# Kernel optimization log

Measured on AMD Instinct MI355X. Metric: run time of the kernel, lower is better.

Reference implementation:

```python
import jax, jax.numpy as jnp
import numpy as np

D_MODEL = 1024
EXPAND = 2
D_EXPAND = D_MODEL * EXPAND  # 2048
D_STATE = 16
DT_RANK = -(-D_MODEL // 16)  # ceil = 64
BATCH = 4
SEQ = 1024


def setup_inputs() -> dict:
    key = jax.random.key(0)
    ks = jax.random.split(key, 9)
    s = 0.02
    x = jax.random.normal(ks[0], (BATCH, SEQ, D_MODEL), dtype=jnp.float32)
    W_in = jax.random.normal(ks[1], (2 * D_EXPAND, D_MODEL), dtype=jnp.float32) * s
    conv_w = jax.random.normal(ks[2], (D_EXPAND, 1, 3), dtype=jnp.float32) * 0.3  # depthwise kernel (O, I/g=1, K)
    conv_b = jax.random.normal(ks[3], (D_EXPAND,), dtype=jnp.float32) * s
    W_xproj = jax.random.normal(ks[4], (2 * D_STATE + DT_RANK, D_EXPAND), dtype=jnp.float32) * s
    dt_std = DT_RANK ** (-0.5) * 0.5
    W_dt = jax.random.uniform(ks[5], (D_EXPAND, DT_RANK), dtype=jnp.float32, minval=-dt_std, maxval=dt_std)
    b_dt = jax.random.normal(ks[6], (D_EXPAND,), dtype=jnp.float32) * s
    A_log = jnp.log(jnp.tile(jnp.arange(1, D_STATE + 1, dtype=jnp.float32), (D_EXPAND, 1)))
    D = jnp.ones((D_EXPAND,), dtype=jnp.float32)
    W_out = jax.random.normal(ks[7], (D_MODEL, D_EXPAND), dtype=jnp.float32) * s
    return {"x": x, "W_in": W_in, "conv_w": conv_w, "conv_b": conv_b,
            "W_xproj": W_xproj, "W_dt": W_dt, "b_dt": b_dt,
            "A_log": A_log, "D": D, "W_out": W_out}


def _mamba_forward(x, W_in, conv_w, conv_b, W_xproj, W_dt, b_dt, A_log, D, W_out):
    B, L, _ = x.shape
    d_exp = D.shape[0]
    n = A_log.shape[1]
    # in_proj -> split into u (ssm branch) and z (gate)
    xz = x @ W_in.T                               # [B, L, 2*d_exp]
    u, z = jnp.split(xz, 2, axis=-1)              # each [B, L, d_exp]
    # depthwise conv1d, kernel 3, padding 1 (same length)
    uc = jax.lax.conv_general_dilated(
        u.transpose(0, 2, 1), conv_w, window_strides=(1,), padding=[(1, 1)],
        feature_group_count=d_exp, dimension_numbers=("NCH", "OIH", "NCH"))
    uc = jax.nn.silu(uc + conv_b[None, :, None]).transpose(0, 2, 1)  # [B, L, d_exp]
    # ssm parameterization
    proj = uc @ W_xproj.T                          # [B, L, 2n + dt_rank]
    B_ssm = proj[..., :n]                          # [B, L, n]
    C_ssm = proj[..., n:2 * n]                     # [B, L, n]
    dt = proj[..., 2 * n:]                         # [B, L, dt_rank]
    delta = jax.nn.softplus(dt @ W_dt.T + b_dt)    # [B, L, d_exp]
    A = -jnp.exp(A_log)                            # [d_exp, n]

    def step(h, inp):
        u_t, d_t, b_t, c_t = inp                   # [B,d], [B,d], [B,n], [B,n]
        dA = jnp.exp(d_t[:, :, None] * A)          # [B, d, n]
        h = dA * h + (d_t * u_t)[:, :, None] * b_t[:, None, :]
        y_t = jnp.einsum("bdn,bn->bd", h, c_t)
        return h, y_t

    xs = (uc.transpose(1, 0, 2), delta.transpose(1, 0, 2),
          B_ssm.transpose(1, 0, 2), C_ssm.transpose(1, 0, 2))
    h0 = jnp.zeros((B, d_exp, n), dtype=uc.dtype)
    _, ys = jax.lax.scan(step, h0, xs)             # ys: [L, B, d_exp]
    y = ys.transpose(1, 0, 2) + uc * D             # skip connection D
    y = y * jax.nn.silu(z)                         # gate
    return y @ W_out.T                             # [B, L, d_model]


def reference(x, W_in, conv_w, conv_b, W_xproj, W_dt, b_dt, A_log, D, W_out):
    return _mamba_forward(x, W_in, conv_w, conv_b, W_xproj, W_dt, b_dt, A_log, D, W_out)
```

## Files before the change

kernel.cpp:

```cpp
#include <hip/hip_runtime.h>
#include <math.h>

#define B_   4
#define L_   1024
#define DM   1024
#define DE   2048
#define NS   16
#define M_   (B_*L_)
#define NC   32
#define CL   32

typedef __attribute__((ext_vector_type(8))) short bf16x8;
typedef __attribute__((ext_vector_type(4))) float f32x4;

#define AS1 __attribute__((address_space(1)))
#define AS3 __attribute__((address_space(3)))

__device__ __forceinline__ void gload_lds16(const void* g, void* l) {
  __builtin_amdgcn_global_load_lds((const AS1 unsigned int*)g,
                                   (AS3 unsigned int*)l, 16, 0, 0);
}

__device__ __forceinline__ unsigned short f2bf(float f) {
  unsigned int u = __builtin_bit_cast(unsigned int, f);
  u = (u + 0x7fffu + ((u >> 16) & 1u)) >> 16;
  return (unsigned short)u;
}
__device__ __forceinline__ float bf2f(unsigned short h) {
  unsigned int u = ((unsigned int)h) << 16;
  return __builtin_bit_cast(float, u);
}
__device__ __forceinline__ float fexp2(float x) {
  return __builtin_amdgcn_exp2f(x);
}

__global__ __launch_bounds__(256)
void convert_all_k(const float* __restrict__ x, const float* __restrict__ Win,
                   const float* __restrict__ Wout, const float* __restrict__ Wx,
                   unsigned short* __restrict__ x_bf, unsigned short* __restrict__ Win_bf,
                   unsigned short* __restrict__ Wout_bf, unsigned short* __restrict__ Wxp) {
  const int blk = blockIdx.x;
  const float* src; unsigned short* dst; size_t base; bool pad = false;
  if (blk < 2048)      { src = x;    dst = x_bf;    base = (size_t)blk * 2048; }
  else if (blk < 4096) { src = Win;  dst = Win_bf;  base = (size_t)(blk - 2048) * 2048; }
  else if (blk < 5120) { src = Wout; dst = Wout_bf; base = (size_t)(blk - 4096) * 2048; }
  else                 { src = Wx;   dst = Wxp;     base = (size_t)(blk - 5120) * 2048; pad = true; }
  const size_t i = base + (size_t)threadIdx.x * 8;
  unsigned short o[8] = {0,0,0,0,0,0,0,0};
  if (!pad || (int)(i >> 11) < 96) {
    float4 a = *(const float4*)(src + i);
    float4 b = *(const float4*)(src + i + 4);
    o[0]=f2bf(a.x); o[1]=f2bf(a.y); o[2]=f2bf(a.z); o[3]=f2bf(a.w);
    o[4]=f2bf(b.x); o[5]=f2bf(b.y); o[6]=f2bf(b.z); o[7]=f2bf(b.w);
  }
  *(ulonglong2*)(dst + i) = *(const ulonglong2*)o;
}

__global__ __launch_bounds__(256, 2)
void gemm1_k(const unsigned short* __restrict__ A, const unsigned short* __restrict__ Bt,
             unsigned short* __restrict__ C) {
  __shared__ unsigned short Asl[256 * 32];
  __shared__ unsigned short Bsl[128 * 32];
  const int tid  = threadIdx.x;
  const int lane = tid & 63;
  const int wave = tid >> 6;
  const int row0 = blockIdx.y * 256, col0 = blockIdx.x * 128;
  const int wr = (wave >> 1) * 128, wc = (wave & 1) * 64;

  const unsigned short* AgP[4];
  #pragma unroll
  for (int g = 0; g < 4; ++g) {
    const int c = g * 256 + tid;
    AgP[g] = A + (size_t)(row0 + (c >> 2)) * DM + ((c & 3) << 3);
  }
  const unsigned short* BgP[2];
  #pragma unroll
  for (int g = 0; g < 2; ++g) {
    const int c = g * 256 + tid;
    BgP[g] = Bt + (size_t)(col0 + (c >> 2)) * DM + ((c & 3) << 3);
  }

  const int frow = lane & 15;
  const int fk   = (lane >> 4) << 3;
  const unsigned short* Afr = Asl + ((wr + frow) << 5) + fk;
  const unsigned short* Bfr = Bsl + ((wc + frow) << 5) + fk;

  f32x4 acc[8][4];
  #pragma unroll
  for (int m = 0; m < 8; ++m)
    #pragma unroll
    for (int n = 0; n < 4; ++n) acc[m][n] = (f32x4){0.f, 0.f, 0.f, 0.f};

  for (int k0 = 0; k0 < DM; k0 += 32) {
    __syncthreads();
    #pragma unroll
    for (int g = 0; g < 4; ++g)
      gload_lds16(AgP[g] + k0, Asl + (((g << 8) + (wave << 6)) << 3));
    #pragma unroll
    for (int g = 0; g < 2; ++g)
      gload_lds16(BgP[g] + k0, Bsl + (((g << 8) + (wave << 6)) << 3));
    __syncthreads();
    bf16x8 af[8], bfr[4];
    #pragma unroll
    for (int m = 0; m < 8; ++m) af[m]  = *(const bf16x8*)(Afr + (m << 9));
    #pragma unroll
    for (int n = 0; n < 4; ++n) bfr[n] = *(const bf16x8*)(Bfr + (n << 9));
    #pragma unroll
    for (int m = 0; m < 8; ++m)
      #pragma unroll
      for (int n = 0; n < 4; ++n)
        acc[m][n] = __builtin_amdgcn_mfma_f32_16x16x32_bf16(af[m], bfr[n], acc[m][n], 0, 0, 0);
  }

  const int r4 = (lane >> 4) << 2;
  #pragma unroll
  for (int m = 0; m < 8; ++m)
    #pragma unroll
    for (int n = 0; n < 4; ++n) {
      unsigned short* Cp = C + (size_t)(row0 + wr + m * 16 + r4) * 4096 + col0 + wc + n * 16 + (lane & 15);
      #pragma unroll
      for (int r = 0; r < 4; ++r) Cp[(size_t)r * 4096] = f2bf(acc[m][n][r]);
    }
}

__global__ __launch_bounds__(256)
void gemm2_k(const unsigned short* __restrict__ A, const unsigned short* __restrict__ Bt,
             float* __restrict__ C) {
  __shared__ unsigned short Asl[128 * 32];
  __shared__ unsigned short Bsl[64 * 32];
  const int tid  = threadIdx.x;
  const int lane = tid & 63;
  const int wave = tid >> 6;
  const int row0 = blockIdx.y * 128, col0 = blockIdx.x * 64;
  const int wr = (wave >> 1) * 64, wc = (wave & 1) * 32;

  const int c0 = tid, c1 = 256 + tid;
  const unsigned short* Ag0 = A + (size_t)(row0 + (c0 >> 2)) * DE + ((c0 & 3) << 3);
  const unsigned short* Ag1 = A + (size_t)(row0 + (c1 >> 2)) * DE + ((c1 & 3) << 3);
  const unsigned short* Bg0 = Bt + (size_t)(col0 + (c0 >> 2)) * DE + ((c0 & 3) << 3);
  unsigned short* Al0 = Asl + ((wave << 6) << 3);
  unsigned short* Al1 = Asl + ((256 + (wave << 6)) << 3);
  unsigned short* Bl0 = Bsl + ((wave << 6) << 3);

  const int frow = lane & 15;
  const int fk   = (lane >> 4) << 3;
  const unsigned short* Afr = Asl + ((wr + frow) << 5) + fk;
  const unsigned short* Bfr = Bsl + ((wc + frow) << 5) + fk;

  f32x4 acc[4][2];
  #pragma unroll
  for (int m = 0; m < 4; ++m)
    #pragma unroll
    for (int n = 0; n < 2; ++n) acc[m][n] = (f32x4){0.f, 0.f, 0.f, 0.f};

  for (int k0 = 0; k0 < DE; k0 += 32) {
    __syncthreads();
    gload_lds16(Ag0 + k0, Al0);
    gload_lds16(Ag1 + k0, Al1);
    gload_lds16(Bg0 + k0, Bl0);
    __syncthreads();
    bf16x8 af[4], bfr[2];
    #pragma unroll
    for (int m = 0; m < 4; ++m) af[m]  = *(const bf16x8*)(Afr + (m << 9));
    #pragma unroll
    for (int n = 0; n < 2; ++n) bfr[n] = *(const bf16x8*)(Bfr + (n << 9));
    #pragma unroll
    for (int m = 0; m < 4; ++m)
      #pragma unroll
      for (int n = 0; n < 2; ++n)
        acc[m][n] = __builtin_amdgcn_mfma_f32_16x16x32_bf16(af[m], bfr[n], acc[m][n], 0, 0, 0);
  }

  const int r4 = (lane >> 4) << 2;
  #pragma unroll
  for (int m = 0; m < 4; ++m)
    #pragma unroll
    for (int n = 0; n < 2; ++n) {
      float* Cp = C + (size_t)(row0 + wr + m * 16 + r4) * DM + col0 + wc + n * 16 + (lane & 15);
      #pragma unroll
      for (int r = 0; r < 4; ++r) Cp[(size_t)r * DM] = acc[m][n][r];
    }
}

__global__ __launch_bounds__(256)
void proj_gemm_k(const unsigned short* __restrict__ A,
                 const unsigned short* __restrict__ Bt,
                 float* __restrict__ part) {
  __shared__ unsigned short Asl[128 * 32];
  __shared__ unsigned short Bsl[128 * 32];
  const int tid  = threadIdx.x;
  const int lane = tid & 63;
  const int wave = tid >> 6;
  const int ks   = blockIdx.x;
  const int row0 = blockIdx.y * 128;
  const int wr = (wave >> 1) * 64, wc = (wave & 1) * 64;
  const int kbase = ks * 256;

  const int c0 = tid, c1 = 256 + tid;
  const unsigned short* Ag0 = A + (size_t)(row0 + (c0 >> 2)) * DE + ((c0 & 3) << 3) + kbase;
  const unsigned short* Ag1 = A + (size_t)(row0 + (c1 >> 2)) * DE + ((c1 & 3) << 3) + kbase;
  const unsigned short* Bg0 = Bt + (size_t)(c0 >> 2) * DE + ((c0 & 3) << 3) + kbase;
  const unsigned short* Bg1 = Bt + (size_t)(c1 >> 2) * DE + ((c1 & 3) << 3) + kbase;
  unsigned short* Al0 = Asl + ((wave << 6) << 3);
  unsigned short* Al1 = Asl + ((256 + (wave << 6)) << 3);
  unsigned short* Bl0 = Bsl + ((wave << 6) << 3);
  unsigned short* Bl1 = Bsl + ((256 + (wave << 6)) << 3);

  const int frow = lane & 15;
  const int fk   = (lane >> 4) << 3;
  const unsigned short* Afr = Asl + ((wr + frow) << 5) + fk;
  const unsigned short* Bfr = Bsl + ((wc + frow) << 5) + fk;

  f32x4 acc[4][4];
  #pragma unroll
  for (int m = 0; m < 4; ++m)
    #pragma unroll
    for (int n = 0; n < 4; ++n) acc[m][n] = (f32x4){0.f, 0.f, 0.f, 0.f};

  for (int k0 = 0; k0 < 256; k0 += 32) {
    __syncthreads();
    gload_lds16(Ag0 + k0, Al0);
    gload_lds16(Ag1 + k0, Al1);
    gload_lds16(Bg0 + k0, Bl0);
    gload_lds16(Bg1 + k0, Bl1);
    __syncthreads();
    bf16x8 af[4], bfr[4];
    #pragma unroll
    for (int m = 0; m < 4; ++m) af[m]  = *(const bf16x8*)(Afr + (m << 9));
    #pragma unroll
    for (int n = 0; n < 4; ++n) bfr[n] = *(const bf16x8*)(Bfr + (n << 9));
    #pragma unroll
    for (int m = 0; m < 4; ++m)
      #pragma unroll
      for (int n = 0; n < 4; ++n)
        acc[m][n] = __builtin_amdgcn_mfma_f32_16x16x32_bf16(af[m], bfr[n], acc[m][n], 0, 0, 0);
  }

  float* Cb = part + (size_t)ks * (M_ * 128) + (size_t)row0 * 128;
  const int r4 = (lane >> 4) << 2;
  #pragma unroll
  for (int m = 0; m < 4; ++m)
    #pragma unroll
    for (int n = 0; n < 4; ++n) {
      float* Cp = Cb + (size_t)(wr + m * 16 + r4) * 128 + wc + n * 16 + (lane & 15);
      #pragma unroll
      for (int r = 0; r < 4; ++r) Cp[(size_t)r * 128] = acc[m][n][r];
    }
}

__global__ __launch_bounds__(256)
void proj_reduce_k(const float* __restrict__ part, float* __restrict__ proj) {
  const int g = blockIdx.x * 256 + threadIdx.x;
  const int m = g / 24;
  const int j4 = (g - m * 24) * 4;
  float4 s = make_float4(0.f, 0.f, 0.f, 0.f);
  #pragma unroll
  for (int ks = 0; ks < 8; ++ks) {
    float4 v = *(const float4*)(part + (size_t)ks * (M_ * 128) + (size_t)m * 128 + j4);
    s.x += v.x; s.y += v.y; s.z += v.z; s.w += v.w;
  }
  *(float4*)(proj + (size_t)m * 96 + j4) = s;
}

__global__ __launch_bounds__(256)
void conv_silu_k(const unsigned short* __restrict__ xz, const float* __restrict__ cw,
                 const float* __restrict__ cb, unsigned short* __restrict__ uc_bf) {
  const int g = blockIdx.x * 256 + threadIdx.x;
  const int m = g >> 9;
  const int d4 = (g & 511) << 2;
  const int l = m & (L_ - 1);
  const unsigned short* row = xz + (size_t)m * 4096 + d4;
  unsigned short cu[4], pv[4] = {0,0,0,0}, nx[4] = {0,0,0,0};
  *(unsigned long long*)cu = *(const unsigned long long*)row;
  if (l > 0)      *(unsigned long long*)pv = *(const unsigned long long*)(row - 4096);
  if (l < L_ - 1) *(unsigned long long*)nx = *(const unsigned long long*)(row + 4096);
  unsigned short ob[4];
  #pragma unroll
  for (int i = 0; i < 4; ++i) {
    const int d = d4 + i;
    float v = cb[d] + cw[d*3]*bf2f(pv[i]) + cw[d*3+1]*bf2f(cu[i]) + cw[d*3+2]*bf2f(nx[i]);
    ob[i] = f2bf(v / (1.f + __expf(-v)));
  }
  *(unsigned long long*)(uc_bf + (size_t)m * DE + d4) = *(const unsigned long long*)ob;
}

__global__ __launch_bounds__(256)
void delta_k(const float* __restrict__ proj, const float* __restrict__ Wdt,
             const float* __restrict__ bdt, unsigned short* __restrict__ dl) {
  __shared__ float As[64][64];
  __shared__ float Bs[64][64];
  const int tid = threadIdx.x;
  const int row0 = blockIdx.y * 64, col0 = blockIdx.x * 64;
  const int ty = tid >> 4, tx = tid & 15;
  #pragma unroll
  for (int q = 0; q < 4; ++q) {
    const int f = q*256 + tid;
    const int rr = f >> 4, cc = (f & 15) << 2;
    float4 v = *(const float4*)(proj + (size_t)(row0+rr)*96 + 32 + cc);
    As[cc+0][rr]=v.x; As[cc+1][rr]=v.y; As[cc+2][rr]=v.z; As[cc+3][rr]=v.w;
    float4 w = *(const float4*)(Wdt + (size_t)(col0+rr)*64 + cc);
    Bs[cc+0][rr]=w.x; Bs[cc+1][rr]=w.y; Bs[cc+2][rr]=w.z; Bs[cc+3][rr]=w.w;
  }
  __syncthreads();
  float acc[4][4];
  #pragma unroll
  for (int i = 0; i < 4; ++i)
    #pragma unroll
    for (int j = 0; j < 4; ++j) acc[i][j] = 0.f;
  #pragma unroll 8
  for (int k = 0; k < 64; ++k) {
    const float4 a = *(const float4*)&As[k][ty*4];
    const float4 w = *(const float4*)&Bs[k][tx*4];
    const float a_[4]={a.x,a.y,a.z,a.w}, b_[4]={w.x,w.y,w.z,w.w};
    #pragma unroll
    for (int i = 0; i < 4; ++i)
      #pragma unroll
      for (int j = 0; j < 4; ++j)
        acc[i][j] = fmaf(a_[i], b_[j], acc[i][j]);
  }
  #pragma unroll
  for (int i = 0; i < 4; ++i) {
    const int m = row0 + ty*4 + i;
    unsigned short ob[4];
    #pragma unroll
    for (int j = 0; j < 4; ++j) {
      const float v = acc[i][j] + bdt[col0 + tx*4 + j];
      ob[j] = f2bf(fmaxf(v, 0.f) + __logf(1.f + __expf(-fabsf(v))));
    }
    *(unsigned long long*)(dl + (size_t)m*DE + col0 + tx*4) = *(const unsigned long long*)ob;
  }
}

__global__ __launch_bounds__(256)
void scan_part1(const unsigned short* __restrict__ dl, const unsigned short* __restrict__ uc,
                const float* __restrict__ proj, const float* __restrict__ Alog,
                float* __restrict__ hX, float* __restrict__ sumdv) {
  __shared__ float Bsh[CL][NS];
  const int tid = threadIdx.x;
  const int d = blockIdx.x * 256 + tid;
  const int c = blockIdx.y;
  const int b = blockIdx.z;
  const size_t mt0 = (size_t)b * L_ + c * CL;
  if (tid < CL * NS / 4) {
    const int t = tid >> 2, n4 = (tid & 3) * 4;
    float4 v = *(const float4*)(proj + (mt0 + t) * 96 + n4);
    Bsh[t][n4] = v.x; Bsh[t][n4+1] = v.y; Bsh[t][n4+2] = v.z; Bsh[t][n4+3] = v.w;
  }
  float An2[NS];
  #pragma unroll
  for (int q = 0; q < 4; ++q) {
    float4 a = *(const float4*)(Alog + d * NS + q * 4);
    An2[q*4+0] = -__expf(a.x) * 1.44269504f;
    An2[q*4+1] = -__expf(a.y) * 1.44269504f;
    An2[q*4+2] = -__expf(a.z) * 1.44269504f;
    An2[q*4+3] = -__expf(a.w) * 1.44269504f;
  }
  __syncthreads();
  float h[NS];
  #pragma unroll
  for (int n = 0; n < NS; ++n) h[n] = 0.f;
  float sd = 0.f;
  size_t off = mt0 * DE + d;
  float dv = bf2f(dl[off]), uv = bf2f(uc[off]);
  for (int t = 0; t < CL; ++t) {
    float dvn = 0.f, uvn = 0.f;
    if (t + 1 < CL) { dvn = bf2f(dl[off + DE]); uvn = bf2f(uc[off + DE]); }
    sd += dv;
    const float du = dv * uv;
    #pragma unroll
    for (int n = 0; n < NS; ++n) {
      const float dA = fexp2(dv * An2[n]);
      h[n] = fmaf(dA, h[n], du * Bsh[t][n]);
    }
    dv = dvn; uv = uvn; off += DE;
  }
  const size_t xb = (size_t)(b * NC + c) * NS * DE + d;
  #pragma unroll
  for (int n = 0; n < NS; ++n) hX[xb + (size_t)n * DE] = h[n];
  sumdv[(size_t)(b * NC + c) * DE + d] = sd;
}

__global__ __launch_bounds__(256)
void scan_combine(float* __restrict__ hX, const float* __restrict__ sumdv,
                  const float* __restrict__ Alog) {
  const int tid = threadIdx.x;
  const int d = blockIdx.x * 256 + tid;
  const int n = blockIdx.y;
  const int b = blockIdx.z;
  const float An2 = -__expf(Alog[d * NS + n]) * 1.44269504f;
  float H = 0.f;
  for (int c = 0; c < NC; ++c) {
    const size_t xi = ((size_t)(b * NC + c) * NS + n) * DE + d;
    const float hf = hX[xi];
    const float sd = sumdv[(size_t)(b * NC + c) * DE + d];
    hX[xi] = H;
    H = fmaf(fexp2(sd * An2), H, hf);
  }
}

__global__ __launch_bounds__(256)
void scan_part2(const unsigned short* __restrict__ dl, const unsigned short* __restrict__ uc,
                const float* __restrict__ proj, const float* __restrict__ hX,
                const float* __restrict__ Alog, const float* __restrict__ Dv,
                const unsigned short* __restrict__ xz, unsigned short* __restrict__ ybf) {
  __shared__ float Bsh[CL][NS];
  __shared__ float Csh[CL][NS];
  const int tid = threadIdx.x;
  const int d = blockIdx.x * 256 + tid;
  const int c = blockIdx.y;
  const int b = blockIdx.z;
  const size_t mt0 = (size_t)b * L_ + c * CL;
  if (tid < 128) {
    const int t = tid >> 2, n4 = (tid & 3) * 4;
    float4 v = *(const float4*)(proj + (mt0 + t) * 96 + n4);
    Bsh[t][n4] = v.x; Bsh[t][n4+1] = v.y; Bsh[t][n4+2] = v.z; Bsh[t][n4+3] = v.w;
  } else {
    const int u = tid - 128;
    const int t = u >> 2, n4 = (u & 3) * 4;
    float4 v = *(const float4*)(proj + (mt0 + t) * 96 + 16 + n4);
    Csh[t][n4] = v.x; Csh[t][n4+1] = v.y; Csh[t][n4+2] = v.z; Csh[t][n4+3] = v.w;
  }
  float An2[NS];
  #pragma unroll
  for (int q = 0; q < 4; ++q) {
    float4 a = *(const float4*)(Alog + d * NS + q * 4);
    An2[q*4+0] = -__expf(a.x) * 1.44269504f;
    An2[q*4+1] = -__expf(a.y) * 1.44269504f;
    An2[q*4+2] = -__expf(a.z) * 1.44269504f;
    An2[q*4+3] = -__expf(a.w) * 1.44269504f;
  }
  const float Dd = Dv[d];
  float h[NS];
  const size_t xb = (size_t)(b * NC + c) * NS * DE + d;
  #pragma unroll
  for (int n = 0; n < NS; ++n) h[n] = hX[xb + (size_t)n * DE];
  __syncthreads();
  size_t off = mt0 * DE + d;
  size_t zoff = mt0 * 4096 + d + 2048;
  float dv = bf2f(dl[off]), uv = bf2f(uc[off]);
  for (int t = 0; t < CL; ++t) {
    float dvn = 0.f, uvn = 0.f;
    if (t + 1 < CL) { dvn = bf2f(dl[off + DE]); uvn = bf2f(uc[off + DE]); }
    const float zv = bf2f(xz[zoff]);
    const float du = dv * uv;
    float y = 0.f;
    #pragma unroll
    for (int n = 0; n < NS; ++n) {
      const float dA = fexp2(dv * An2[n]);
      h[n] = fmaf(dA, h[n], du * Bsh[t][n]);
      y = fmaf(h[n], Csh[t][n], y);
    }
    y = fmaf(uv, Dd, y);
    const float sz = zv / (1.f + __expf(-zv));
    ybf[off] = f2bf(y * sz);
    dv = dvn; uv = uvn; off += DE; zoff += 4096;
  }
}

extern "C" void kernel_launch(void* const* d_in, const int* in_sizes, int n_in,
                              void* d_out, int out_size, void* d_ws, size_t ws_size,
                              hipStream_t stream) {
  const float* x    = (const float*)d_in[0];
  const float* Win  = (const float*)d_in[1];
  const float* cw   = (const float*)d_in[2];
  const float* cb   = (const float*)d_in[3];
  const float* Wx   = (const float*)d_in[4];
  const float* Wdt  = (const float*)d_in[5];
  const float* bdt  = (const float*)d_in[6];
  const float* Alog = (const float*)d_in[7];
  const float* Dv   = (const float*)d_in[8];
  const float* Wout = (const float*)d_in[9];
  float* out = (float*)d_out;
  float* ws  = (float*)d_ws;

  unsigned short* xz_bf   = (unsigned short*)(ws);
  float*          proj    = ws + 8388608;
  float*          hX      = ws + 8781824;
  float*          part    = hX;
  float*          sumdv   = ws + 12976128;
  unsigned short* x_bf    = (unsigned short*)(ws + 13238272);
  unsigned short* Win_bf  = (unsigned short*)(ws + 15335424);
  unsigned short* Wout_bf = (unsigned short*)(ws + 17432576);
  unsigned short* Wxp_bf  = (unsigned short*)(ws + 18481152);
  unsigned short* uc_bf   = (unsigned short*)(ws + 18612224);
  unsigned short* y_bf    = uc_bf;
  unsigned short* dl_bf   = (unsigned short*)(ws + 22806528);

  convert_all_k<<<5248, 256, 0, stream>>>(x, Win, Wout, Wx, x_bf, Win_bf, Wout_bf, Wxp_bf);
  gemm1_k<<<dim3(32, 16), 256, 0, stream>>>(x_bf, Win_bf, xz_bf);
  conv_silu_k<<<8192, 256, 0, stream>>>(xz_bf, cw, cb, uc_bf);
  proj_gemm_k<<<dim3(8, 32), 256, 0, stream>>>(uc_bf, Wxp_bf, part);
  proj_reduce_k<<<384, 256, 0, stream>>>(part, proj);
  delta_k<<<dim3(32, 64), 256, 0, stream>>>(proj, Wdt, bdt, dl_bf);
  scan_part1<<<dim3(DE/256, NC, B_), 256, 0, stream>>>(dl_bf, uc_bf, proj, Alog, hX, sumdv);
  scan_combine<<<dim3(DE/256, NS, B_), 256, 0, stream>>>(hX, sumdv, Alog);
  scan_part2<<<dim3(DE/256, NC, B_), 256, 0, stream>>>(dl_bf, uc_bf, proj, hX, Alog, Dv, xz_bf, y_bf);
  gemm2_k<<<dim3(16, 32), 256, 0, stream>>>(y_bf, Wout_bf, out);
}
```

Before: 206.6 us.

## Double GEMM K-tile to 64 with XOR-swizzled LDS and split scan reduction

In both bf16 MFMA GEMMs, each K tile grows from 32 to 64 elements, so each block runs half as many barrier-separated load/compute iterations. The LDS layout is XOR-swizzled on 16-byte chunks by row, which is meant to avoid bank conflicts on the fragment reads. The scan kernel splits the y dot product across four partial accumulators to shorten its dependent FMA chain. The cost is twice the LDS per block, which may lower occupancy in gemm1 since it requests 2 blocks per CU.

```diff
diff --git a/kernel.cpp b/kernel.cpp
--- a/kernel.cpp
+++ b/kernel.cpp
@@ -59,31 +59,32 @@
 __global__ __launch_bounds__(256, 2)
 void gemm1_k(const unsigned short* __restrict__ A, const unsigned short* __restrict__ Bt,
              unsigned short* __restrict__ C) {
-  __shared__ unsigned short Asl[256 * 32];
-  __shared__ unsigned short Bsl[128 * 32];
+  __shared__ unsigned short Asl[256 * 64];
+  __shared__ unsigned short Bsl[128 * 64];
   const int tid  = threadIdx.x;
   const int lane = tid & 63;
   const int wave = tid >> 6;
   const int row0 = blockIdx.y * 256, col0 = blockIdx.x * 128;
   const int wr = (wave >> 1) * 128, wc = (wave & 1) * 64;
 
-  const unsigned short* AgP[4];
+  const unsigned short* AgP[8];
+  #pragma unroll
+  for (int g = 0; g < 8; ++g) {
+    const int c = g * 256 + tid, r = c >> 3;
+    AgP[g] = A + (size_t)(row0 + r) * DM + ((((c & 7) ^ (r & 7)) << 3));
+  }
+  const unsigned short* BgP[4];
   #pragma unroll
   for (int g = 0; g < 4; ++g) {
-    const int c = g * 256 + tid;
-    AgP[g] = A + (size_t)(row0 + (c >> 2)) * DM + ((c & 3) << 3);
-  }
-  const unsigned short* BgP[2];
-  #pragma unroll
-  for (int g = 0; g < 2; ++g) {
-    const int c = g * 256 + tid;
-    BgP[g] = Bt + (size_t)(col0 + (c >> 2)) * DM + ((c & 3) << 3);
+    const int c = g * 256 + tid, r = c >> 3;
+    BgP[g] = Bt + (size_t)(col0 + r) * DM + ((((c & 7) ^ (r & 7)) << 3));
   }
 
   const int frow = lane & 15;
   const int fk   = (lane >> 4) << 3;
-  const unsigned short* Afr = Asl + ((wr + frow) << 5) + fk;
-  const unsigned short* Bfr = Bsl + ((wc + frow) << 5) + fk;
+  const int sA0  = fk ^ ((frow & 7) << 3);
+  const unsigned short* Afr = Asl + (wr + frow) * 64;
+  const unsigned short* Bfr = Bsl + (wc + frow) * 64;
 
   f32x4 acc[8][4];
   #pragma unroll
@@ -91,25 +92,29 @@
     #pragma unroll
     for (int n = 0; n < 4; ++n) acc[m][n] = (f32x4){0.f, 0.f, 0.f, 0.f};
 
-  for (int k0 = 0; k0 < DM; k0 += 32) {
+  for (int k0 = 0; k0 < DM; k0 += 64) {
     __syncthreads();
     #pragma unroll
+    for (int g = 0; g < 8; ++g)
+      gload_lds16(AgP[g] + k0, Asl + (((g << 8) + (wave << 6)) << 3));
+    #pragma unroll
     for (int g = 0; g < 4; ++g)
-      gload_lds16(AgP[g] + k0, Asl + (((g << 8) + (wave << 6)) << 3));
-    #pragma unroll
-    for (int g = 0; g < 2; ++g)
       gload_lds16(BgP[g] + k0, Bsl + (((g << 8) + (wave << 6)) << 3));
     __syncthreads();
-    bf16x8 af[8], bfr[4];
-    #pragma unroll
-    for (int m = 0; m < 8; ++m) af[m]  = *(const bf16x8*)(Afr + (m << 9));
-    #pragma unroll
-    for (int n = 0; n < 4; ++n) bfr[n] = *(const bf16x8*)(Bfr + (n << 9));
-    #pragma unroll
-    for (int m = 0; m < 8; ++m)
-      #pragma unroll
-      for (int n = 0; n < 4; ++n)
-        acc[m][n] = __builtin_amdgcn_mfma_f32_16x16x32_bf16(af[m], bfr[n], acc[m][n], 0, 0, 0);
+    #pragma unroll
+    for (int kk = 0; kk < 2; ++kk) {
+      const int so = sA0 ^ (kk << 5);
+      bf16x8 af[8], bfr[4];
+      #pragma unroll
+      for (int m = 0; m < 8; ++m) af[m]  = *(const bf16x8*)(Afr + (m << 10) + so);
+      #pragma unroll
+      for (int n = 0; n < 4; ++n) bfr[n] = *(const bf16x8*)(Bfr + (n << 10) + so);
+      #pragma unroll
+      for (int m = 0; m < 8; ++m)
+        #pragma unroll
+        for (int n = 0; n < 4; ++n)
+          acc[m][n] = __builtin_amdgcn_mfma_f32_16x16x32_bf16(af[m], bfr[n], acc[m][n], 0, 0, 0);
+    }
   }
 
   const int r4 = (lane >> 4) << 2;
@@ -126,26 +131,32 @@
 __global__ __launch_bounds__(256)
 void gemm2_k(const unsigned short* __restrict__ A, const unsigned short* __restrict__ Bt,
              float* __restrict__ C) {
-  __shared__ unsigned short Asl[128 * 32];
-  __shared__ unsigned short Bsl[64 * 32];
+  __shared__ unsigned short Asl[128 * 64];
+  __shared__ unsigned short Bsl[64 * 64];
   const int tid  = threadIdx.x;
   const int lane = tid & 63;
   const int wave = tid >> 6;
   const int row0 = blockIdx.y * 128, col0 = blockIdx.x * 64;
   const int wr = (wave >> 1) * 64, wc = (wave & 1) * 32;
 
-  const int c0 = tid, c1 = 256 + tid;
-  const unsigned short* Ag0 = A + (size_t)(row0 + (c0 >> 2)) * DE + ((c0 & 3) << 3);
-  const unsigned short* Ag1 = A + (size_t)(row0 + (c1 >> 2)) * DE + ((c1 & 3) << 3);
-  const unsigned short* Bg0 = Bt + (size_t)(col0 + (c0 >> 2)) * DE + ((c0 & 3) << 3);
-  unsigned short* Al0 = Asl + ((wave << 6) << 3);
-  unsigned short* Al1 = Asl + ((256 + (wave << 6)) << 3);
-  unsigned short* Bl0 = Bsl + ((wave << 6) << 3);
+  const unsigned short* AgP[4];
+  #pragma unroll
+  for (int g = 0; g < 4; ++g) {
+    const int c = g * 256 + tid, r = c >> 3;
+    AgP[g] = A + (size_t)(row0 + r) * DE + ((((c & 7) ^ (r & 7)) << 3));
+  }
+  const unsigned short* BgP[2];
+  #pragma unroll
+  for (int g = 0; g < 2; ++g) {
+    const int c = g * 256 + tid, r = c >> 3;
+    BgP[g] = Bt + (size_t)(col0 + r) * DE + ((((c & 7) ^ (r & 7)) << 3));
+  }
 
   const int frow = lane & 15;
   const int fk   = (lane >> 4) << 3;
-  const unsigned short* Afr = Asl + ((wr + frow) << 5) + fk;
-  const unsigned short* Bfr = Bsl + ((wc + frow) << 5) + fk;
+  const int sA0  = fk ^ ((frow & 7) << 3);
+  const unsigned short* Afr = Asl + (wr + frow) * 64;
+  const unsigned short* Bfr = Bsl + (wc + frow) * 64;
 
   f32x4 acc[4][2];
   #pragma unroll
@@ -153,22 +164,29 @@
     #pragma unroll
     for (int n = 0; n < 2; ++n) acc[m][n] = (f32x4){0.f, 0.f, 0.f, 0.f};
 
-  for (int k0 = 0; k0 < DE; k0 += 32) {
+  for (int k0 = 0; k0 < DE; k0 += 64) {
     __syncthreads();
-    gload_lds16(Ag0 + k0, Al0);
-    gload_lds16(Ag1 + k0, Al1);
-    gload_lds16(Bg0 + k0, Bl0);
+    #pragma unroll
+    for (int g = 0; g < 4; ++g)
+      gload_lds16(AgP[g] + k0, Asl + (((g << 8) + (wave << 6)) << 3));
+    #pragma unroll
+    for (int g = 0; g < 2; ++g)
+      gload_lds16(BgP[g] + k0, Bsl + (((g << 8) + (wave << 6)) << 3));
     __syncthreads();
-    bf16x8 af[4], bfr[2];
-    #pragma unroll
-    for (int m = 0; m < 4; ++m) af[m]  = *(const bf16x8*)(Afr + (m << 9));
-    #pragma unroll
-    for (int n = 0; n < 2; ++n) bfr[n] = *(const bf16x8*)(Bfr + (n << 9));
-    #pragma unroll
-    for (int m = 0; m < 4; ++m)
-      #pragma unroll
-      for (int n = 0; n < 2; ++n)
-        acc[m][n] = __builtin_amdgcn_mfma_f32_16x16x32_bf16(af[m], bfr[n], acc[m][n], 0, 0, 0);
+    #pragma unroll
+    for (int kk = 0; kk < 2; ++kk) {
+      const int so = sA0 ^ (kk << 5);
+      bf16x8 af[4], bfr[2];
+      #pragma unroll
+      for (int m = 0; m < 4; ++m) af[m]  = *(const bf16x8*)(Afr + (m << 10) + so);
+      #pragma unroll
+      for (int n = 0; n < 2; ++n) bfr[n] = *(const bf16x8*)(Bfr + (n << 10) + so);
+      #pragma unroll
+      for (int m = 0; m < 4; ++m)
+        #pragma unroll
+        for (int n = 0; n < 2; ++n)
+          acc[m][n] = __builtin_amdgcn_mfma_f32_16x16x32_bf16(af[m], bfr[n], acc[m][n], 0, 0, 0);
+    }
   }
 
   const int r4 = (lane >> 4) << 2;
@@ -443,13 +461,14 @@
     if (t + 1 < CL) { dvn = bf2f(dl[off + DE]); uvn = bf2f(uc[off + DE]); }
     const float zv = bf2f(xz[zoff]);
     const float du = dv * uv;
-    float y = 0.f;
+    float yp[4] = {0.f, 0.f, 0.f, 0.f};
     #pragma unroll
     for (int n = 0; n < NS; ++n) {
       const float dA = fexp2(dv * An2[n]);
       h[n] = fmaf(dA, h[n], du * Bsh[t][n]);
-      y = fmaf(h[n], Csh[t][n], y);
-    }
+      yp[n & 3] = fmaf(h[n], Csh[t][n], yp[n & 3]);
+    }
+    float y = (yp[0] + yp[1]) + (yp[2] + yp[3]);
     y = fmaf(uv, Dd, y);
     const float sz = zv / (1.f + __expf(-zv));
     ybf[off] = f2bf(y * sz);
```

Result: faster. 198.5 us (-3.9%).
